# Optimization experiments

Hardware: AMD Instinct MI355X
Metric: run time of the kernel (lower is better)

The kernel has to match this reference:

```python
import jax, jax.numpy as jnp
import numpy as np

N, B, LMAX, DIM, IMG_DIM, LY, H = 32768, 16, 2560, 512, 768, 256, 8


def _layernorm(x, g, b, eps=1e-5):
    mu = jnp.mean(x, axis=-1, keepdims=True)
    var = jnp.mean(jnp.square(x - mu), axis=-1, keepdims=True)
    return (x - mu) * jax.lax.rsqrt(var + eps) * g + b


def setup_inputs() -> dict:
    key = jax.random.key(0)
    ks = jax.random.split(key, 16)
    s = DIM ** -0.5
    # ragged per-batch counts summing to N, all <= LMAX
    counts = np.full(B, N // B, dtype=np.int64)
    counts[: B // 2] += 200
    counts[B // 2:] -= 200
    batch_ids = jnp.asarray(np.repeat(np.arange(B), counts), dtype=jnp.int32)
    return {
        "F": jax.random.normal(ks[0], (N, DIM), jnp.float32),
        "y": jax.random.normal(ks[1], (B, LY, IMG_DIM), jnp.float32),
        "ln_g": jnp.ones((DIM,), jnp.float32),
        "ln_b": jnp.zeros((DIM,), jnp.float32),
        "Wq": jax.random.normal(ks[2], (DIM, DIM), jnp.float32) * s,
        "Wk": jax.random.normal(ks[3], (DIM, DIM), jnp.float32) * s,
        "Wv": jax.random.normal(ks[4], (DIM, DIM), jnp.float32) * s,
        "bq": jnp.zeros((DIM,), jnp.float32),
        "bk": jnp.zeros((DIM,), jnp.float32),
        "bv": jnp.zeros((DIM,), jnp.float32),
        "Wo": jax.random.normal(ks[5], (DIM, DIM), jnp.float32) * s,
        "bo": jnp.zeros((DIM,), jnp.float32),
        "W1": jax.random.normal(ks[6], (DIM, IMG_DIM), jnp.float32) * (IMG_DIM ** -0.5),
        "b1": jnp.zeros((DIM,), jnp.float32),
        "W2": jax.random.normal(ks[7], (DIM, DIM), jnp.float32) * s,
        "b2": jnp.zeros((DIM,), jnp.float32),
        "batch_ids": batch_ids,
        "Lmax": LMAX,
    }


def reference(F, y, ln_g, ln_b, Wq, Wk, Wv, bq, bk, bv, Wo, bo, W1, b1, W2, b2, batch_ids, Lmax):
    Bb, Ly, _ = y.shape
    n, dim = F.shape
    dh = dim // H
    # sparse -> dense: per-token slot index within its batch (batch_ids sorted)
    offsets = jnp.searchsorted(batch_ids, jnp.arange(Bb, dtype=batch_ids.dtype))
    pos = jnp.arange(n, dtype=jnp.int32) - offsets[batch_ids].astype(jnp.int32)
    xd = jnp.zeros((Bb, Lmax, dim), F.dtype).at[batch_ids, pos].set(F)  # [B,Lmax,D]
    # NOTE: self.norm is re-bound in subclass => same LayerNorm used twice
    xd = _layernorm(xd, ln_g, ln_b)
    # MLP fuse of image features: Linear -> GELU(exact) -> Linear
    ym = jax.nn.gelu(y @ W1.T + b1, approximate=False) @ W2.T + b2  # [B,Ly,D]
    # MHA cross-attention (no key_padding_mask: mask arg defaults to None)
    q = (xd @ Wq.T + bq).reshape(Bb, Lmax, H, dh)
    k = (ym @ Wk.T + bk).reshape(Bb, Ly, H, dh)
    v = (ym @ Wv.T + bv).reshape(Bb, Ly, H, dh)
    scores = jnp.einsum("bqhd,bkhd->bhqk", q, k) * (dh ** -0.5)
    attn = jax.nn.softmax(scores, axis=-1)
    o = jnp.einsum("bhqk,bkhd->bqhd", attn, v).reshape(Bb, Lmax, dim)
    o = o @ Wo.T + bo
    out_dense = _layernorm(xd + o, ln_g, ln_b)
    # dense -> sparse gather (equivalent to x_dense[x_mask])
    return out_dense[batch_ids, pos]
```

## Files before the change

kernel.cpp:

```cpp
#include <hip/hip_runtime.h>
#include <stdint.h>

#define NTOK 32768
#define BD   512
#define NB   16
#define LYK  256
#define IMGD 768

typedef __attribute__((ext_vector_type(4))) float f32x4;
typedef __attribute__((ext_vector_type(8))) short s16x8;
typedef __attribute__((ext_vector_type(4))) unsigned short u16x4;
typedef unsigned short u16;

__device__ __forceinline__ float bf2f(u16 u) {
  union { uint32_t i; float f; } v; v.i = ((uint32_t)u) << 16; return v.f;
}
__device__ __forceinline__ u16 f2bf(float f) {
  union { float f; uint32_t i; } v; v.f = f;
  uint32_t r = v.i + 0x7fffu + ((v.i >> 16) & 1u);
  return (u16)(r >> 16);
}
__device__ __forceinline__ void gl_lds16(const u16* g, u16* l) {
  __builtin_amdgcn_global_load_lds(
      (const __attribute__((address_space(1))) uint32_t*)g,
      (__attribute__((address_space(3))) uint32_t*)l, 16, 0, 0);
}
__device__ __forceinline__ f32x4 mfma16(s16x8 a, s16x8 b, f32x4 c) {
  return __builtin_amdgcn_mfma_f32_16x16x32_bf16(a, b, c, 0, 0, 0);
}

__global__ __launch_bounds__(256) void prep(
    const float* __restrict__ wq, const float* __restrict__ wk,
    const float* __restrict__ wv, const float* __restrict__ wo,
    const float* __restrict__ w2, const float* __restrict__ w1,
    const float* __restrict__ y,  const float* __restrict__ F,
    const float* __restrict__ g,  const float* __restrict__ be,
    const int* __restrict__ bids,
    u16* __restrict__ dq, u16* __restrict__ dkv, u16* __restrict__ dwo,
    u16* __restrict__ dw2, u16* __restrict__ dw1, u16* __restrict__ dy,
    u16* __restrict__ xn, int* __restrict__ off) {
  const int bid = blockIdx.x;
  if (bid < 2368) {
    const float* s; u16* d; int base;
    if      (bid < 128)  { s = wq; d = dq;            base = 0;   }
    else if (bid < 256)  { s = wk; d = dkv;           base = 128; }
    else if (bid < 384)  { s = wv; d = dkv + 262144;  base = 256; }
    else if (bid < 512)  { s = wo; d = dwo;           base = 384; }
    else if (bid < 640)  { s = w2; d = dw2;           base = 512; }
    else if (bid < 832)  { s = w1; d = dw1;           base = 640; }
    else                 { s = y;  d = dy;            base = 832; }
    int i = ((bid - base) * 256 + threadIdx.x) * 8;
    f32x4 a = *(const f32x4*)(s + i);
    f32x4 b = *(const f32x4*)(s + i + 4);
    s16x8 o;
#pragma unroll
    for (int j = 0; j < 4; ++j) { o[j] = (short)f2bf(a[j]); o[4 + j] = (short)f2bf(b[j]); }
    *(s16x8*)(d + i) = o;
  } else if (bid < 10560) {
    const int lane = threadIdx.x & 63;
    const size_t row = (size_t)(bid - 2368) * 4 + (threadIdx.x >> 6);
    const float* x = F + row * BD + lane * 8;
    f32x4 a = *(const f32x4*)x;
    f32x4 b = *(const f32x4*)(x + 4);
    float v[8] = {a[0], a[1], a[2], a[3], b[0], b[1], b[2], b[3]};
    float s = 0.f, s2 = 0.f;
#pragma unroll
    for (int j = 0; j < 8; ++j) { s += v[j]; s2 += v[j] * v[j]; }
#pragma unroll
    for (int m = 1; m < 64; m <<= 1) { s += __shfl_xor(s, m); s2 += __shfl_xor(s2, m); }
    float mean = s * (1.f / BD);
    float rstd = rsqrtf(s2 * (1.f / BD) - mean * mean + 1e-5f);
    const float* gp = g + lane * 8;
    const float* bp = be + lane * 8;
    s16x8 o;
#pragma unroll
    for (int j = 0; j < 8; ++j) o[j] = (short)f2bf((v[j] - mean) * rstd * gp[j] + bp[j]);
    *(s16x8*)(xn + row * BD + lane * 8) = o;
  } else {
    int b = threadIdx.x;
    if (b > NB) return;
    int lo = 0, hi = NTOK;
    while (lo < hi) { int mid = (lo + hi) >> 1; if (bids[mid] < b) lo = mid + 1; else hi = mid; }
    off[b] = lo;
  }
}

__global__ __launch_bounds__(256) void ln_bf16_f32(const u16* __restrict__ Z,
                                                   const float* __restrict__ g,
                                                   const float* __restrict__ be,
                                                   float* __restrict__ out) {
  const int lane = threadIdx.x & 63;
  const size_t row = (size_t)blockIdx.x * 4 + (threadIdx.x >> 6);
  s16x8 zv = *(const s16x8*)(Z + row * BD + lane * 8);
  float v[8];
#pragma unroll
  for (int j = 0; j < 8; ++j) v[j] = bf2f((u16)zv[j]);
  float s = 0.f, s2 = 0.f;
#pragma unroll
  for (int j = 0; j < 8; ++j) { s += v[j]; s2 += v[j] * v[j]; }
#pragma unroll
  for (int m = 1; m < 64; m <<= 1) { s += __shfl_xor(s, m); s2 += __shfl_xor(s2, m); }
  float mean = s * (1.f / BD);
  float rstd = rsqrtf(s2 * (1.f / BD) - mean * mean + 1e-5f);
  const float* gp = g + lane * 8;
  const float* bp = be + lane * 8;
  f32x4 o0, o1;
#pragma unroll
  for (int j = 0; j < 4; ++j) o0[j] = (v[j] - mean) * rstd * gp[j] + bp[j];
#pragma unroll
  for (int j = 0; j < 4; ++j) o1[j] = (v[4 + j] - mean) * rstd * gp[4 + j] + bp[4 + j];
  float* op = out + row * BD + lane * 8;
  *(f32x4*)op = o0;
  *(f32x4*)(op + 4) = o1;
}

template <int TM, int EPI, int SWZ>
__global__ __launch_bounds__(256, 2) void gemm_nt(const u16* __restrict__ A,
                                                  const u16* __restrict__ W,
                                                  const float* __restrict__ bias,
                                                  u16* __restrict__ C,
                                                  const u16* __restrict__ resid,
                                                  u16* __restrict__ C2,
                                                  const float* __restrict__ bias2,
                                                  int K) {
  constexpr int MT = 4;
  constexpr int NT = (TM == 128) ? 4 : 2;
  __shared__ u16 As[TM * 32];
  __shared__ u16 Bs[128 * 32];
  const int tid = threadIdx.x;
  const int wave = tid >> 6, lane = tid & 63;
  const int wm = (TM == 128) ? (wave & 1) * 64 : 0;
  const int wn = (TM == 128) ? (wave >> 1) * 64 : wave * 32;
  const int quad = lane >> 4, l16 = lane & 15;
  int m_t, n_t;
  if (SWZ) {
    const int bid = blockIdx.x;
    const int xcd = bid & 7, j = bid >> 3;
    n_t = j & 3;
    m_t = xcd + (j >> 2) * 8;
  } else {
    m_t = blockIdx.x; n_t = blockIdx.y;
  }
  const int m0 = m_t * TM, n0 = n_t * 128;

  f32x4 acc[MT][NT];
#pragma unroll
  for (int i = 0; i < MT; ++i)
#pragma unroll
    for (int j = 0; j < NT; ++j) acc[i][j] = f32x4{0.f, 0.f, 0.f, 0.f};

  const int scol = (lane & 3) * 8;
  const int srowA = (TM == 128) ? wave * 32 + (lane >> 2) : wave * 16 + (lane >> 2);
  const int srowB = wave * 32 + (lane >> 2);
  const u16* gA0 = A + (size_t)(m0 + srowA) * K + scol;
  const u16* gA1 = gA0 + (size_t)16 * K;
  const u16* gW0 = W + (size_t)(n0 + srowB) * K + scol;
  const u16* gW1 = gW0 + (size_t)16 * K;
  u16* lA = As + ((TM == 128) ? wave * 1024 : wave * 512);
  u16* lB = Bs + wave * 1024;

  for (int k0 = 0; k0 < K; k0 += 32) {
    __syncthreads();
    gl_lds16(gA0 + k0, lA);
    if (TM == 128) gl_lds16(gA1 + k0, lA + 512);
    gl_lds16(gW0 + k0, lB);
    gl_lds16(gW1 + k0, lB + 512);
    __syncthreads();
    s16x8 af[MT], bfr[NT];
#pragma unroll
    for (int mt = 0; mt < MT; ++mt)
      af[mt] = *(const s16x8*)&As[(wm + mt * 16 + l16) * 32 + quad * 8];
#pragma unroll
    for (int nt = 0; nt < NT; ++nt)
      bfr[nt] = *(const s16x8*)&Bs[(wn + nt * 16 + l16) * 32 + quad * 8];
#pragma unroll
    for (int mt = 0; mt < MT; ++mt)
#pragma unroll
      for (int nt = 0; nt < NT; ++nt)
        acc[mt][nt] = mfma16(af[mt], bfr[nt], acc[mt][nt]);
  }

#pragma unroll
  for (int nt = 0; nt < NT; ++nt) {
    const int n = n0 + wn + nt * 16 + l16;
    const float bia = (EPI == 3) ? (n < BD ? bias[n] : bias2[n - BD]) : bias[n];
#pragma unroll
    for (int mt = 0; mt < MT; ++mt) {
      const int mb = m0 + wm + mt * 16 + quad * 4;
      if (EPI == 3 && n >= BD) {
        u16x4 pk;
#pragma unroll
        for (int r = 0; r < 4; ++r) pk[r] = f2bf(acc[mt][nt][r] + bia);
        const int b = mb >> 8, k0i = mb & 255;
        *(u16x4*)&C2[((size_t)b * BD + (n - BD)) * LYK + k0i] = pk;
      } else {
#pragma unroll
        for (int r = 0; r < 4; ++r) {
          float v = acc[mt][nt][r] + bia;
          size_t idx = (size_t)(mb + r) * BD + n;
          if (EPI == 1) v = 0.5f * v * (1.f + erff(v * 0.70710678118654752f));
          if (EPI == 2) v += bf2f(resid[idx]);
          C[idx] = f2bf(v);
        }
      }
    }
  }
}

__global__ __launch_bounds__(256, 2) void attn_k(const u16* __restrict__ Q,
                                                 const u16* __restrict__ Kg,
                                                 const u16* __restrict__ VT,
                                                 const int* __restrict__ off,
                                                 u16* __restrict__ O) {
  const int t = blockIdx.x, h = blockIdx.y, b = blockIdx.z;
  const int qend = off[b + 1];
  const int qstart = off[b] + t * 64;
  if (qstart >= qend) return;

  __shared__ u16 VTs[64 * 264];
  __shared__ u16 Ps[4 * 16 * 264];

  const int tid = threadIdx.x;
  const int wave = tid >> 6, lane = tid & 63;
  const int quad = lane >> 4, l16 = lane & 15;

  const u16* vsrc = VT + ((size_t)b * BD + h * 64) * LYK;
#pragma unroll
  for (int s = 0; s < 8; ++s) {
    int seg = tid + s * 256;
    int r = seg >> 5, c = (seg & 31) * 8;
    *(s16x8*)&VTs[r * 264 + c] = *(const s16x8*)&vsrc[(size_t)r * LYK + c];
  }

  int qrow = qstart + wave * 16 + l16;
  if (qrow > NTOK - 1) qrow = NTOK - 1;
  const u16* qp = Q + (size_t)qrow * BD + h * 64 + quad * 8;
  s16x8 aq0 = *(const s16x8*)qp;
  s16x8 aq1 = *(const s16x8*)(qp + 32);

  const u16* kb = Kg + (size_t)b * LYK * BD + h * 64;
  f32x4 sacc[16];
#pragma unroll
  for (int nt = 0; nt < 16; ++nt) sacc[nt] = f32x4{0.f, 0.f, 0.f, 0.f};
#pragma unroll
  for (int nt = 0; nt < 16; ++nt) {
    const u16* kp = kb + (size_t)(nt * 16 + l16) * BD + quad * 8;
    s16x8 b0 = *(const s16x8*)kp;
    s16x8 b1 = *(const s16x8*)(kp + 32);
    sacc[nt] = mfma16(aq0, b0, sacc[nt]);
    sacc[nt] = mfma16(aq1, b1, sacc[nt]);
  }

  float inv[4];
#pragma unroll
  for (int r = 0; r < 4; ++r) {
    float m = -1e30f;
#pragma unroll
    for (int nt = 0; nt < 16; ++nt) m = fmaxf(m, sacc[nt][r]);
#pragma unroll
    for (int msk = 1; msk < 16; msk <<= 1) m = fmaxf(m, __shfl_xor(m, msk));
    float sum = 0.f;
#pragma unroll
    for (int nt = 0; nt < 16; ++nt) {
      float p = __expf(0.125f * (sacc[nt][r] - m));
      sacc[nt][r] = p;
      sum += p;
    }
#pragma unroll
    for (int msk = 1; msk < 16; msk <<= 1) sum += __shfl_xor(sum, msk);
    inv[r] = 1.f / sum;
  }

  u16* Pw = Ps + wave * (16 * 264);
#pragma unroll
  for (int nt = 0; nt < 16; ++nt)
#pragma unroll
    for (int r = 0; r < 4; ++r)
      Pw[(quad * 4 + r) * 264 + nt * 16 + l16] = f2bf(sacc[nt][r]);

  __syncthreads();

  f32x4 oacc[4];
#pragma unroll
  for (int n2 = 0; n2 < 4; ++n2) oacc[n2] = f32x4{0.f, 0.f, 0.f, 0.f};
#pragma unroll
  for (int kc = 0; kc < 8; ++kc) {
    s16x8 ap = *(const s16x8*)&Pw[l16 * 264 + kc * 32 + quad * 8];
#pragma unroll
    for (int n2 = 0; n2 < 4; ++n2) {
      s16x8 bv = *(const s16x8*)&VTs[(n2 * 16 + l16) * 264 + kc * 32 + quad * 8];
      oacc[n2] = mfma16(ap, bv, oacc[n2]);
    }
  }

#pragma unroll
  for (int n2 = 0; n2 < 4; ++n2)
#pragma unroll
    for (int r = 0; r < 4; ++r) {
      int q = qstart + wave * 16 + quad * 4 + r;
      if (q < qend)
        O[(size_t)q * BD + h * 64 + n2 * 16 + l16] = f2bf(oacc[n2][r] * inv[r]);
    }
}

extern "C" void kernel_launch(void* const* d_in, const int* in_sizes, int n_in,
                              void* d_out, int out_size, void* d_ws, size_t ws_size,
                              hipStream_t stream) {
  const float* F    = (const float*)d_in[0];
  const float* yIn  = (const float*)d_in[1];
  const float* ln_g = (const float*)d_in[2];
  const float* ln_b = (const float*)d_in[3];
  const float* Wq   = (const float*)d_in[4];
  const float* Wk   = (const float*)d_in[5];
  const float* Wv   = (const float*)d_in[6];
  const float* bq   = (const float*)d_in[7];
  const float* bk   = (const float*)d_in[8];
  const float* bv   = (const float*)d_in[9];
  const float* Wo   = (const float*)d_in[10];
  const float* bo   = (const float*)d_in[11];
  const float* W1   = (const float*)d_in[12];
  const float* b1   = (const float*)d_in[13];
  const float* W2   = (const float*)d_in[14];
  const float* b2   = (const float*)d_in[15];
  const int* bids   = (const int*)d_in[16];

  char* ws = (char*)d_ws;
  size_t cur = 0;
  auto alloc = [&](size_t bytes) {
    void* p = ws + cur;
    cur += (bytes + 255) & ~(size_t)255;
    return p;
  };

  int* off   = (int*)alloc(68);
  u16* wq_b  = (u16*)alloc((size_t)262144 * 2);
  u16* wkv_b = (u16*)alloc((size_t)524288 * 2);
  u16* wo_b  = (u16*)alloc((size_t)262144 * 2);
  u16* w2_b  = (u16*)alloc((size_t)262144 * 2);
  u16* w1_b  = (u16*)alloc((size_t)393216 * 2);
  u16* y_b   = (u16*)alloc((size_t)3145728 * 2);
  u16* U     = (u16*)alloc((size_t)4096 * BD * 2);
  u16* ym    = (u16*)alloc((size_t)4096 * BD * 2);
  u16* Kb    = (u16*)alloc((size_t)4096 * BD * 2);
  u16* VT    = (u16*)alloc((size_t)NB * BD * LYK * 2);
  u16* xn    = (u16*)alloc((size_t)NTOK * BD * 2);
  u16* Qb    = (u16*)alloc((size_t)NTOK * BD * 2);
  u16* Ob    = (u16*)alloc((size_t)NTOK * BD * 2);
  u16* Zb    = (u16*)alloc((size_t)NTOK * BD * 2);

  prep<<<10561, 256, 0, stream>>>(Wq, Wk, Wv, Wo, W2, W1, yIn, F, ln_g, ln_b, bids,
                                  wq_b, wkv_b, wo_b, w2_b, w1_b, y_b, xn, off);

  gemm_nt<64, 1, 0><<<dim3(64, 4), 256, 0, stream>>>(y_b, w1_b, b1, U, nullptr, nullptr, nullptr, IMGD);
  gemm_nt<64, 0, 0><<<dim3(64, 4), 256, 0, stream>>>(U, w2_b, b2, ym, nullptr, nullptr, nullptr, BD);
  gemm_nt<128, 3, 0><<<dim3(32, 8), 256, 0, stream>>>(ym, wkv_b, bk, Kb, nullptr, VT, bv, BD);
  gemm_nt<128, 0, 1><<<1024, 256, 0, stream>>>(xn, wq_b, bq, Qb, nullptr, nullptr, nullptr, BD);
  attn_k<<<dim3(36, 8, NB), 256, 0, stream>>>(Qb, Kb, VT, off, Ob);
  gemm_nt<128, 2, 1><<<1024, 256, 0, stream>>>(Ob, wo_b, bo, Zb, xn, nullptr, nullptr, BD);
  ln_bf16_f32<<<NTOK / 4, 256, 0, stream>>>(Zb, ln_g, ln_b, (float*)d_out);
}
```

Before: 395.4 us.

## Deepen GEMM K-step to 64 and stage K in LDS with transposed scores

```diff
diff --git a/kernel.cpp b/kernel.cpp
--- a/kernel.cpp
+++ b/kernel.cpp
@@ -19,6 +19,10 @@
   union { float f; uint32_t i; } v; v.f = f;
   uint32_t r = v.i + 0x7fffu + ((v.i >> 16) & 1u);
   return (u16)(r >> 16);
+}
+__device__ __forceinline__ u16 f2bf_fast(float f) {
+  union { float f; uint32_t i; } v; v.f = f;
+  return (u16)((v.i + 0x8000u) >> 16);
 }
 __device__ __forceinline__ void gl_lds16(const u16* g, u16* l) {
   __builtin_amdgcn_global_load_lds(
@@ -114,8 +118,71 @@
   *(f32x4*)(op + 4) = o1;
 }
 
-template <int TM, int EPI, int SWZ>
-__global__ __launch_bounds__(256, 2) void gemm_nt(const u16* __restrict__ A,
+template <int EPI>
+__global__ __launch_bounds__(256, 2) void gemm64(const u16* __restrict__ A,
+                                                 const u16* __restrict__ W,
+                                                 const float* __restrict__ bias,
+                                                 u16* __restrict__ C, int K) {
+  __shared__ u16 As[64 * 32];
+  __shared__ u16 Bs[128 * 32];
+  const int tid = threadIdx.x;
+  const int wave = tid >> 6, lane = tid & 63;
+  const int wn = wave * 32;
+  const int quad = lane >> 4, l16 = lane & 15;
+  const int m0 = blockIdx.x * 64, n0 = blockIdx.y * 128;
+
+  f32x4 acc[4][2];
+#pragma unroll
+  for (int i = 0; i < 4; ++i)
+#pragma unroll
+    for (int j = 0; j < 2; ++j) acc[i][j] = f32x4{0.f, 0.f, 0.f, 0.f};
+
+  const int scol = (lane & 3) * 8;
+  const u16* gA0 = A + (size_t)(m0 + wave * 16 + (lane >> 2)) * K + scol;
+  const u16* gW0 = W + (size_t)(n0 + wave * 32 + (lane >> 2)) * K + scol;
+  const u16* gW1 = gW0 + (size_t)16 * K;
+  u16* lA = As + wave * 512;
+  u16* lB = Bs + wave * 1024;
+
+  for (int k0 = 0; k0 < K; k0 += 32) {
+    __syncthreads();
+    gl_lds16(gA0 + k0, lA);
+    gl_lds16(gW0 + k0, lB);
+    gl_lds16(gW1 + k0, lB + 512);
+    __syncthreads();
+    s16x8 af[4], bfr[2];
+#pragma unroll
+    for (int mt = 0; mt < 4; ++mt)
+      af[mt] = *(const s16x8*)&As[(mt * 16 + l16) * 32 + quad * 8];
+#pragma unroll
+    for (int nt = 0; nt < 2; ++nt)
+      bfr[nt] = *(const s16x8*)&Bs[(wn + nt * 16 + l16) * 32 + quad * 8];
+#pragma unroll
+    for (int mt = 0; mt < 4; ++mt)
+#pragma unroll
+      for (int nt = 0; nt < 2; ++nt)
+        acc[mt][nt] = mfma16(af[mt], bfr[nt], acc[mt][nt]);
+  }
+
+#pragma unroll
+  for (int nt = 0; nt < 2; ++nt) {
+    const int n = n0 + wn + nt * 16 + l16;
+    const float bia = bias[n];
+#pragma unroll
+    for (int mt = 0; mt < 4; ++mt) {
+      const int mb = m0 + mt * 16 + quad * 4;
+#pragma unroll
+      for (int r = 0; r < 4; ++r) {
+        float v = acc[mt][nt][r] + bia;
+        if (EPI == 1) v = 0.5f * v * (1.f + erff(v * 0.70710678118654752f));
+        C[(size_t)(mb + r) * BD + n] = f2bf(v);
+      }
+    }
+  }
+}
+
+template <int EPI, int SWZ>
+__global__ __launch_bounds__(256, 2) void gemm128(const u16* __restrict__ A,
                                                   const u16* __restrict__ W,
                                                   const float* __restrict__ bias,
                                                   u16* __restrict__ C,
@@ -123,14 +190,11 @@
                                                   u16* __restrict__ C2,
                                                   const float* __restrict__ bias2,
                                                   int K) {
-  constexpr int MT = 4;
-  constexpr int NT = (TM == 128) ? 4 : 2;
-  __shared__ u16 As[TM * 32];
-  __shared__ u16 Bs[128 * 32];
+  __shared__ u16 As[128 * 64];
+  __shared__ u16 Bs[128 * 64];
   const int tid = threadIdx.x;
   const int wave = tid >> 6, lane = tid & 63;
-  const int wm = (TM == 128) ? (wave & 1) * 64 : 0;
-  const int wn = (TM == 128) ? (wave >> 1) * 64 : wave * 32;
+  const int wm = (wave & 1) * 64, wn = (wave >> 1) * 64;
   const int quad = lane >> 4, l16 = lane & 15;
   int m_t, n_t;
   if (SWZ) {
@@ -141,51 +205,54 @@
   } else {
     m_t = blockIdx.x; n_t = blockIdx.y;
   }
-  const int m0 = m_t * TM, n0 = n_t * 128;
-
-  f32x4 acc[MT][NT];
-#pragma unroll
-  for (int i = 0; i < MT; ++i)
-#pragma unroll
-    for (int j = 0; j < NT; ++j) acc[i][j] = f32x4{0.f, 0.f, 0.f, 0.f};
-
-  const int scol = (lane & 3) * 8;
-  const int srowA = (TM == 128) ? wave * 32 + (lane >> 2) : wave * 16 + (lane >> 2);
-  const int srowB = wave * 32 + (lane >> 2);
-  const u16* gA0 = A + (size_t)(m0 + srowA) * K + scol;
-  const u16* gA1 = gA0 + (size_t)16 * K;
-  const u16* gW0 = W + (size_t)(n0 + srowB) * K + scol;
-  const u16* gW1 = gW0 + (size_t)16 * K;
-  u16* lA = As + ((TM == 128) ? wave * 1024 : wave * 512);
-  u16* lB = Bs + wave * 1024;
-
-  for (int k0 = 0; k0 < K; k0 += 32) {
+  const int m0 = m_t * 128, n0 = n_t * 128;
+
+  f32x4 acc[4][4];
+#pragma unroll
+  for (int i = 0; i < 4; ++i)
+#pragma unroll
+    for (int j = 0; j < 4; ++j) acc[i][j] = f32x4{0.f, 0.f, 0.f, 0.f};
+
+  const int srow = wave * 32 + (lane >> 3);
+  const int scol = (lane & 7) * 8;
+  const u16* gA = A + (size_t)(m0 + srow) * K + scol;
+  const u16* gW = W + (size_t)(n0 + srow) * K + scol;
+  u16* lA = As + wave * 2048;
+  u16* lB = Bs + wave * 2048;
+
+  for (int k0 = 0; k0 < K; k0 += 64) {
     __syncthreads();
-    gl_lds16(gA0 + k0, lA);
-    if (TM == 128) gl_lds16(gA1 + k0, lA + 512);
-    gl_lds16(gW0 + k0, lB);
-    gl_lds16(gW1 + k0, lB + 512);
+#pragma unroll
+    for (int s = 0; s < 4; ++s) gl_lds16(gA + (size_t)s * 8 * K + k0, lA + s * 512);
+#pragma unroll
+    for (int s = 0; s < 4; ++s) gl_lds16(gW + (size_t)s * 8 * K + k0, lB + s * 512);
     __syncthreads();
-    s16x8 af[MT], bfr[NT];
-#pragma unroll
-    for (int mt = 0; mt < MT; ++mt)
-      af[mt] = *(const s16x8*)&As[(wm + mt * 16 + l16) * 32 + quad * 8];
-#pragma unroll
-    for (int nt = 0; nt < NT; ++nt)
-      bfr[nt] = *(const s16x8*)&Bs[(wn + nt * 16 + l16) * 32 + quad * 8];
-#pragma unroll
-    for (int mt = 0; mt < MT; ++mt)
-#pragma unroll
-      for (int nt = 0; nt < NT; ++nt)
-        acc[mt][nt] = mfma16(af[mt], bfr[nt], acc[mt][nt]);
-  }
-
-#pragma unroll
-  for (int nt = 0; nt < NT; ++nt) {
+    s16x8 af[4][2], bfr[4][2];
+#pragma unroll
+    for (int mt = 0; mt < 4; ++mt)
+#pragma unroll
+      for (int ks = 0; ks < 2; ++ks)
+        af[mt][ks] = *(const s16x8*)&As[(wm + mt * 16 + l16) * 64 + ks * 32 + quad * 8];
+#pragma unroll
+    for (int nt = 0; nt < 4; ++nt)
+#pragma unroll
+      for (int ks = 0; ks < 2; ++ks)
+        bfr[nt][ks] = *(const s16x8*)&Bs[(wn + nt * 16 + l16) * 64 + ks * 32 + quad * 8];
+#pragma unroll
+    for (int ks = 0; ks < 2; ++ks)
+#pragma unroll
+      for (int mt = 0; mt < 4; ++mt)
+#pragma unroll
+        for (int nt = 0; nt < 4; ++nt)
+          acc[mt][nt] = mfma16(af[mt][ks], bfr[nt][ks], acc[mt][nt]);
+  }
+
+#pragma unroll
+  for (int nt = 0; nt < 4; ++nt) {
     const int n = n0 + wn + nt * 16 + l16;
     const float bia = (EPI == 3) ? (n < BD ? bias[n] : bias2[n - BD]) : bias[n];
 #pragma unroll
-    for (int mt = 0; mt < MT; ++mt) {
+    for (int mt = 0; mt < 4; ++mt) {
       const int mb = m0 + wm + mt * 16 + quad * 4;
       if (EPI == 3 && n >= BD) {
         u16x4 pk;
@@ -198,7 +265,6 @@
         for (int r = 0; r < 4; ++r) {
           float v = acc[mt][nt][r] + bia;
           size_t idx = (size_t)(mb + r) * BD + n;
-          if (EPI == 1) v = 0.5f * v * (1.f + erff(v * 0.70710678118654752f));
           if (EPI == 2) v += bf2f(resid[idx]);
           C[idx] = f2bf(v);
         }
@@ -217,75 +283,89 @@
   const int qstart = off[b] + t * 64;
   if (qstart >= qend) return;
 
+  __shared__ u16 KT[256 * 72];
   __shared__ u16 VTs[64 * 264];
-  __shared__ u16 Ps[4 * 16 * 264];
 
   const int tid = threadIdx.x;
   const int wave = tid >> 6, lane = tid & 63;
   const int quad = lane >> 4, l16 = lane & 15;
 
-  const u16* vsrc = VT + ((size_t)b * BD + h * 64) * LYK;
-#pragma unroll
-  for (int s = 0; s < 8; ++s) {
-    int seg = tid + s * 256;
-    int r = seg >> 5, c = (seg & 31) * 8;
-    *(s16x8*)&VTs[r * 264 + c] = *(const s16x8*)&vsrc[(size_t)r * LYK + c];
-  }
-
+  {
+    const u16* src = Kg + (size_t)b * LYK * BD + h * 64;
+#pragma unroll
+    for (int s = 0; s < 8; ++s) {
+      int c = tid + s * 256;
+      int r = c >> 3, col = (c & 7) * 8;
+      *(s16x8*)&KT[r * 72 + col] = *(const s16x8*)&src[(size_t)r * BD + col];
+    }
+  }
+  {
+    const u16* src = VT + ((size_t)b * BD + h * 64) * LYK;
+#pragma unroll
+    for (int s = 0; s < 8; ++s) {
+      int c = tid + s * 256;
+      int r = c >> 5, col = (c & 31) * 8;
+      *(s16x8*)&VTs[r * 264 + col] = *(const s16x8*)&src[(size_t)r * LYK + col];
+    }
+  }
   int qrow = qstart + wave * 16 + l16;
   if (qrow > NTOK - 1) qrow = NTOK - 1;
   const u16* qp = Q + (size_t)qrow * BD + h * 64 + quad * 8;
   s16x8 aq0 = *(const s16x8*)qp;
   s16x8 aq1 = *(const s16x8*)(qp + 32);
 
-  const u16* kb = Kg + (size_t)b * LYK * BD + h * 64;
+  __syncthreads();
+
   f32x4 sacc[16];
 #pragma unroll
   for (int nt = 0; nt < 16; ++nt) sacc[nt] = f32x4{0.f, 0.f, 0.f, 0.f};
 #pragma unroll
   for (int nt = 0; nt < 16; ++nt) {
-    const u16* kp = kb + (size_t)(nt * 16 + l16) * BD + quad * 8;
-    s16x8 b0 = *(const s16x8*)kp;
-    s16x8 b1 = *(const s16x8*)(kp + 32);
-    sacc[nt] = mfma16(aq0, b0, sacc[nt]);
-    sacc[nt] = mfma16(aq1, b1, sacc[nt]);
-  }
-
-  float inv[4];
-#pragma unroll
-  for (int r = 0; r < 4; ++r) {
-    float m = -1e30f;
-#pragma unroll
-    for (int nt = 0; nt < 16; ++nt) m = fmaxf(m, sacc[nt][r]);
-#pragma unroll
-    for (int msk = 1; msk < 16; msk <<= 1) m = fmaxf(m, __shfl_xor(m, msk));
-    float sum = 0.f;
-#pragma unroll
-    for (int nt = 0; nt < 16; ++nt) {
-      float p = __expf(0.125f * (sacc[nt][r] - m));
+    const u16* kp = &KT[(nt * 16 + l16) * 72 + quad * 8];
+    s16x8 k0 = *(const s16x8*)kp;
+    s16x8 k1 = *(const s16x8*)(kp + 32);
+    sacc[nt] = mfma16(k0, aq0, sacc[nt]);
+    sacc[nt] = mfma16(k1, aq1, sacc[nt]);
+  }
+
+  float mx = -1e30f;
+#pragma unroll
+  for (int nt = 0; nt < 16; ++nt)
+#pragma unroll
+    for (int r = 0; r < 4; ++r) mx = fmaxf(mx, sacc[nt][r]);
+  mx = fmaxf(mx, __shfl_xor(mx, 16));
+  mx = fmaxf(mx, __shfl_xor(mx, 32));
+  float sum = 0.f;
+#pragma unroll
+  for (int nt = 0; nt < 16; ++nt)
+#pragma unroll
+    for (int r = 0; r < 4; ++r) {
+      float p = __expf(0.125f * (sacc[nt][r] - mx));
       sacc[nt][r] = p;
       sum += p;
     }
-#pragma unroll
-    for (int msk = 1; msk < 16; msk <<= 1) sum += __shfl_xor(sum, msk);
-    inv[r] = 1.f / sum;
-  }
-
-  u16* Pw = Ps + wave * (16 * 264);
-#pragma unroll
-  for (int nt = 0; nt < 16; ++nt)
-#pragma unroll
-    for (int r = 0; r < 4; ++r)
-      Pw[(quad * 4 + r) * 264 + nt * 16 + l16] = f2bf(sacc[nt][r]);
+  sum += __shfl_xor(sum, 16);
+  sum += __shfl_xor(sum, 32);
+  const float inv = 1.f / sum;
 
   __syncthreads();
 
+  u16* P = KT;
+  const int prow = (wave * 16 + l16) * 264;
+#pragma unroll
+  for (int nt = 0; nt < 16; ++nt) {
+    u16x4 pk;
+#pragma unroll
+    for (int r = 0; r < 4; ++r) pk[r] = f2bf_fast(sacc[nt][r] * inv);
+    *(u16x4*)&P[prow + nt * 16 + quad * 4] = pk;
+  }
+
   f32x4 oacc[4];
 #pragma unroll
   for (int n2 = 0; n2 < 4; ++n2) oacc[n2] = f32x4{0.f, 0.f, 0.f, 0.f};
 #pragma unroll
   for (int kc = 0; kc < 8; ++kc) {
-    s16x8 ap = *(const s16x8*)&Pw[l16 * 264 + kc * 32 + quad * 8];
+    s16x8 ap = *(const s16x8*)&P[prow + kc * 32 + quad * 8];
 #pragma unroll
     for (int n2 = 0; n2 < 4; ++n2) {
       s16x8 bv = *(const s16x8*)&VTs[(n2 * 16 + l16) * 264 + kc * 32 + quad * 8];
@@ -299,7 +379,7 @@
     for (int r = 0; r < 4; ++r) {
       int q = qstart + wave * 16 + quad * 4 + r;
       if (q < qend)
-        O[(size_t)q * BD + h * 64 + n2 * 16 + l16] = f2bf(oacc[n2][r] * inv[r]);
+        O[(size_t)q * BD + h * 64 + n2 * 16 + l16] = f2bf(oacc[n2][r]);
     }
 }
 
@@ -351,11 +431,11 @@
   prep<<<10561, 256, 0, stream>>>(Wq, Wk, Wv, Wo, W2, W1, yIn, F, ln_g, ln_b, bids,
                                   wq_b, wkv_b, wo_b, w2_b, w1_b, y_b, xn, off);
 
-  gemm_nt<64, 1, 0><<<dim3(64, 4), 256, 0, stream>>>(y_b, w1_b, b1, U, nullptr, nullptr, nullptr, IMGD);
-  gemm_nt<64, 0, 0><<<dim3(64, 4), 256, 0, stream>>>(U, w2_b, b2, ym, nullptr, nullptr, nullptr, BD);
-  gemm_nt<128, 3, 0><<<dim3(32, 8), 256, 0, stream>>>(ym, wkv_b, bk, Kb, nullptr, VT, bv, BD);
-  gemm_nt<128, 0, 1><<<1024, 256, 0, stream>>>(xn, wq_b, bq, Qb, nullptr, nullptr, nullptr, BD);
+  gemm64<1><<<dim3(64, 4), 256, 0, stream>>>(y_b, w1_b, b1, U, IMGD);
+  gemm64<0><<<dim3(64, 4), 256, 0, stream>>>(U, w2_b, b2, ym, BD);
+  gemm128<3, 0><<<dim3(32, 8), 256, 0, stream>>>(ym, wkv_b, bk, Kb, nullptr, VT, bv, BD);
+  gemm128<0, 1><<<1024, 256, 0, stream>>>(xn, wq_b, bq, Qb, nullptr, nullptr, nullptr, BD);
   attn_k<<<dim3(36, 8, NB), 256, 0, stream>>>(Qb, Kb, VT, off, Ob);
-  gemm_nt<128, 2, 1><<<1024, 256, 0, stream>>>(Ob, wo_b, bo, Zb, xn, nullptr, nullptr, BD);
+  gemm128<2, 1><<<1024, 256, 0, stream>>>(Ob, wo_b, bo, Zb, xn, nullptr, nullptr, BD);
   ln_bf16_f32<<<NTOK / 4, 256, 0, stream>>>(Zb, ln_g, ln_b, (float*)d_out);
 }
```

Measured after the change: 366.0 us. 1.08x faster.
